# Kernel optimization log

Measured on AMD Instinct MI355X. Metric: run time of the kernel, lower is better.

Reference implementation:

```python
import jax, jax.numpy as jnp
import numpy as np

D = 64        # inner_feature_len (dim)
HID = 128     # hidden_channels of the edge MLP
NCONV = 2     # n_conv
STEPS = 3     # Set2Set processing_steps
NSEG = 128    # number of graphs in the batch


def setup_inputs() -> dict:
    key = jax.random.key(0)
    ks = jax.random.split(key, 30)
    N, E, FN, FE = 10000, 64000, 92, 41
    s = 0.05
    p = lambda i, shape: jax.random.normal(ks[i], shape, jnp.float32) * s
    return {
        "x": jax.random.normal(ks[0], (N, FN), jnp.float32),
        "edge_attr": jax.random.uniform(ks[1], (E, FE), dtype=jnp.float32),
        "lin0_w": p(2, (D, FN)), "lin0_b": p(3, (D,)),
        "nn1_w": p(4, (HID, FE)), "nn1_b": p(5, (HID,)),
        "nn2_w": p(6, (D * D, HID)), "nn2_b": p(7, (D * D,)),
        "root_w": p(8, (D, D)), "conv_b": p(9, (D,)),
        "gru_w_ih": p(10, (3 * D, D)), "gru_w_hh": p(11, (3 * D, D)),
        "gru_b_ih": p(12, (3 * D,)), "gru_b_hh": p(13, (3 * D,)),
        "lstm_w_ih": p(14, (4 * D, 2 * D)), "lstm_w_hh": p(15, (4 * D, D)),
        "lstm_b_ih": p(16, (4 * D,)), "lstm_b_hh": p(17, (4 * D,)),
        "lin1_w": p(18, (D, 2 * D)), "lin1_b": p(19, (D,)),
        "lin2_w": p(20, (1, D)), "lin2_b": p(21, (1,)),
        "edge_index": jax.random.randint(ks[22], (2, E), 0, N, dtype=jnp.int32),
        "batch": jnp.sort(jax.random.randint(ks[23], (N,), 0, NSEG, dtype=jnp.int32)),
    }


def _gru_step(m, h, w_ih, w_hh, b_ih, b_hh):
    # torch GRU gate order: r, z, n
    gi = m @ w_ih.T + b_ih
    gh = h @ w_hh.T + b_hh
    r = jax.nn.sigmoid(gi[:, :D] + gh[:, :D])
    z = jax.nn.sigmoid(gi[:, D:2 * D] + gh[:, D:2 * D])
    n = jnp.tanh(gi[:, 2 * D:] + r * gh[:, 2 * D:])
    return (1.0 - z) * n + z * h


def _forward(x, edge_attr, lin0_w, lin0_b, nn1_w, nn1_b, nn2_w, nn2_b, root_w, conv_b,
             gru_w_ih, gru_w_hh, gru_b_ih, gru_b_hh, lstm_w_ih, lstm_w_hh, lstm_b_ih,
             lstm_b_hh, lin1_w, lin1_b, lin2_w, lin2_b, edge_index, batch):
    N = x.shape[0]
    src, dst = edge_index[0], edge_index[1]

    # Edge-conditioned weight matrices: [E, D, D] (dominant intermediate)
    We = (jax.nn.relu(edge_attr @ nn1_w.T + nn1_b) @ nn2_w.T + nn2_b).reshape(-1, D, D)
    deg = jnp.clip(jax.ops.segment_sum(jnp.ones_like(src, jnp.float32), dst, num_segments=N), 1.0, None)

    out = jax.nn.relu(x @ lin0_w.T + lin0_b)   # [N, D]
    h = out                                     # GRU hidden (num_layers=1)
    for _ in range(NCONV):
        # NNConv: gather -> per-edge matmul -> scatter-mean, plus root transform + bias
        msg = jnp.einsum('ei,eio->eo', out[src], We)                 # [E, D]
        agg = jax.ops.segment_sum(msg, dst, num_segments=N) / deg[:, None]
        m = jax.nn.relu(agg + out @ root_w.T + conv_b)
        h = _gru_step(m, h, gru_w_ih, gru_w_hh, gru_b_ih, gru_b_hh)
        out = h

    # Set2Set pooling (LSTM-attention readout)
    q_star = jnp.zeros((NSEG, 2 * D), x.dtype)
    hl = jnp.zeros((NSEG, D), x.dtype)
    cl = jnp.zeros((NSEG, D), x.dtype)
    for _ in range(STEPS):
        g = q_star @ lstm_w_ih.T + lstm_b_ih + hl @ lstm_w_hh.T + lstm_b_hh
        i = jax.nn.sigmoid(g[:, :D])
        f = jax.nn.sigmoid(g[:, D:2 * D])
        gg = jnp.tanh(g[:, 2 * D:3 * D])
        o = jax.nn.sigmoid(g[:, 3 * D:])
        cl = f * cl + i * gg
        hl = o * jnp.tanh(cl)
        q = hl                                   # [NSEG, D]
        e = jnp.sum(out * q[batch], axis=-1)     # [N]
        mmax = jax.ops.segment_max(e, batch, num_segments=NSEG)
        a = jnp.exp(e - mmax[batch])
        denom = jax.ops.segment_sum(a, batch, num_segments=NSEG)
        a = a / denom[batch]
        r = jax.ops.segment_sum(a[:, None] * out, batch, num_segments=NSEG)  # [NSEG, D]
        q_star = jnp.concatenate([q, r], axis=1)

    y = jax.nn.relu(q_star @ lin1_w.T + lin1_b) @ lin2_w.T + lin2_b
    return y.reshape(-1)


def reference(x, edge_attr, lin0_w, lin0_b, nn1_w, nn1_b, nn2_w, nn2_b, root_w, conv_b,
              gru_w_ih, gru_w_hh, gru_b_ih, gru_b_hh, lstm_w_ih, lstm_w_hh, lstm_b_ih,
              lstm_b_hh, lin1_w, lin1_b, lin2_w, lin2_b, edge_index, batch):
    return _forward(x, edge_attr, lin0_w, lin0_b, nn1_w, nn1_b, nn2_w, nn2_b, root_w,
                    conv_b, gru_w_ih, gru_w_hh, gru_b_ih, gru_b_hh, lstm_w_ih, lstm_w_hh,
                    lstm_b_ih, lstm_b_hh, lin1_w, lin1_b, lin2_w, lin2_b, edge_index, batch)
```

## Files before the change

kernel.cpp:

```cpp
#include <hip/hip_runtime.h>
#include <hip/hip_bf16.h>
#include <math.h>

#define DD 64
#define HIDC 128
#define FN 92
#define FE 41
#define S2CAP 192

typedef unsigned short u16;
typedef short bf16x8 __attribute__((ext_vector_type(8)));
typedef float f32x4 __attribute__((ext_vector_type(4)));
typedef u16 u16x8 __attribute__((ext_vector_type(8)));

__device__ __forceinline__ float sigmoidf_(float x){ return 1.f/(1.f+expf(-x)); }

__device__ __forceinline__ u16 f2bf(float v){
  union { float f; unsigned u; } x; x.f = v;
  unsigned r = x.u + 0x7fff + ((x.u >> 16) & 1);
  return (u16)(r >> 16);
}
__device__ __forceinline__ float bf2f(u16 v){
  union { float f; unsigned u; } x; x.u = ((unsigned)v) << 16;
  return x.f;
}
__device__ __forceinline__ void split_bf(float v, u16& h, u16& l){
  h = f2bf(v); l = f2bf(v - bf2f(h));
}

__global__ void k_pack(const float* __restrict__ lin0_w, const float* __restrict__ nn1_w,
                       const float* __restrict__ root_w, const float* __restrict__ gwih,
                       const float* __restrict__ gwhh, const float* __restrict__ lwih,
                       const float* __restrict__ lwhh, const float* __restrict__ lin1_w,
                       float* __restrict__ lin0T, float* __restrict__ nn1T,
                       float* __restrict__ rootT, float* __restrict__ wihT,
                       float* __restrict__ whhT, float* __restrict__ lwihT,
                       float* __restrict__ lwhhT, float* __restrict__ lin1T)
{
  int idx = blockIdx.x*blockDim.x + threadIdx.x;
  if (idx < 92*64){ int k=idx/64, o=idx%64; lin0T[k*64+o] = lin0_w[o*92+k]; return; } idx -= 92*64;
  if (idx < 41*128){ int k=idx/128, h=idx%128; nn1T[k*128+h] = nn1_w[h*41+k]; return; } idx -= 41*128;
  if (idx < 64*64){ int i=idx/64, o=idx%64; rootT[i*64+o] = root_w[o*64+i]; return; } idx -= 64*64;
  if (idx < 64*192){ int i=idx/192, g=idx%192; wihT[i*192+g] = gwih[g*64+i]; return; } idx -= 64*192;
  if (idx < 64*192){ int i=idx/192, g=idx%192; whhT[i*192+g] = gwhh[g*64+i]; return; } idx -= 64*192;
  if (idx < 128*256){ int j=idx/256, t=idx%256; lwihT[j*256+t] = lwih[t*128+j]; return; } idx -= 128*256;
  if (idx < 64*256){ int j=idx/256, t=idx%256; lwhhT[j*256+t] = lwhh[t*64+j]; return; } idx -= 64*256;
  if (idx < 128*64){ int j=idx/64, t=idx%64; lin1T[j*64+t] = lin1_w[t*128+j]; return; }
}

__global__ void k_pack_b2(const float* __restrict__ nn2_w,
                          u16* __restrict__ BhT, u16* __restrict__ BlT){
  int idx = blockIdx.x*256 + threadIdx.x;
  if (idx >= 524288) return;
  int i  = idx & 63;
  int ho = (idx >> 6) & 4095;
  int c  = idx >> 18;
  int h = ho >> 6, o = ho & 63;
  float v = nn2_w[(size_t)(i*64+o)*128 + c*64 + h];
  u16 hi, lo; split_bf(v, hi, lo);
  BhT[idx] = hi; BlT[idx] = lo;
}

__global__ void k_pack_b1(const float* __restrict__ nn1_w,
                          u16* __restrict__ BT1h, u16* __restrict__ BT1l){
  int idx = blockIdx.x*256 + threadIdx.x;
  if (idx >= 8192) return;
  int h = idx >> 6, k = idx & 63;
  float v = (k < FE) ? nn1_w[(size_t)h*FE + k] : 0.f;
  u16 hi, lo; split_bf(v, hi, lo);
  BT1h[idx] = hi; BT1l[idx] = lo;
}

__global__ void k_split_ea(const float* __restrict__ ea, const int* __restrict__ sortedE,
                           u16* __restrict__ eaH, u16* __restrict__ eaL, int E){
  int idx = blockIdx.x*256 + threadIdx.x;
  if (idx >= E*64) return;
  int ew = idx >> 6, k = idx & 63;
  int e = sortedE[ew];
  float v = (k < FE) ? ea[(size_t)e*FE + k] : 0.f;
  u16 hi, lo; split_bf(v, hi, lo);
  eaH[idx] = hi; eaL[idx] = lo;
}

__global__ __launch_bounds__(256) void k_node_mlp(const float* __restrict__ x,
    const float* __restrict__ lin0T, const float* __restrict__ lin0_b,
    const float* __restrict__ nn2_b,
    float* __restrict__ out, u16* __restrict__ outH, u16* __restrict__ outL,
    float* __restrict__ bterm, int N)
{
  __shared__ float xs[16][FN];
  const int w = threadIdx.x>>6, o = threadIdx.x&63;
  const int nb = blockIdx.x*16 + w*4;
  for (int idx = o; idx < 4*FN; idx += 64){
    int j = idx/FN, k = idx%FN;
    int n = nb + j;
    xs[w*4+j][k] = (n<N) ? x[(size_t)n*FN + k] : 0.f;
  }
  float acc[4];
  float bv = lin0_b[o];
  #pragma unroll
  for (int j=0;j<4;j++) acc[j] = bv;
  for (int k=0;k<FN;k++){
    float lw = lin0T[k*64+o];
    #pragma unroll
    for (int j=0;j<4;j++) acc[j] = fmaf(xs[w*4+j][k], lw, acc[j]);
  }
  float v[4];
  #pragma unroll
  for (int j=0;j<4;j++){
    v[j] = fmaxf(acc[j], 0.f);
    int n = nb + j;
    if (n < N){
      out[(size_t)n*64+o] = v[j];
      u16 hi, lo; split_bf(v[j], hi, lo);
      outH[(size_t)n*64+o] = hi;
      outL[(size_t)n*64+o] = lo;
    }
  }
  float bt[4] = {0.f,0.f,0.f,0.f};
  for (int i=0;i<64;i++){
    float wnb = nn2_b[i*64+o];
    #pragma unroll
    for (int j=0;j<4;j++) bt[j] = fmaf(__shfl(v[j], i, 64), wnb, bt[j]);
  }
  #pragma unroll
  for (int j=0;j<4;j++){
    int n = nb + j;
    if (n < N) bterm[(size_t)n*64+o] = bt[j];
  }
}

__global__ void k_count(const int* __restrict__ dst, const int* __restrict__ src,
                        float* __restrict__ deg, int* __restrict__ scnt, int E){
  int e = blockIdx.x*blockDim.x + threadIdx.x;
  if (e < E){
    atomicAdd(&deg[dst[e]], 1.f);
    atomicAdd(&scnt[src[e]], 1);
  }
}

__global__ void k_scan1(const int* __restrict__ cnt, int* __restrict__ excl,
                        int* __restrict__ bsum, int N){
  __shared__ int buf[256];
  int i = blockIdx.x*256 + threadIdx.x;
  int v = (i<N) ? cnt[i] : 0;
  buf[threadIdx.x] = v;
  __syncthreads();
  #pragma unroll
  for (int off=1; off<256; off<<=1){
    int t = (threadIdx.x>=off) ? buf[threadIdx.x-off] : 0;
    __syncthreads();
    buf[threadIdx.x] += t;
    __syncthreads();
  }
  if (i<N) excl[i] = buf[threadIdx.x] - v;
  if (threadIdx.x==255) bsum[blockIdx.x] = buf[255];
}
__global__ void k_scan2(int* __restrict__ bsum, int nb){
  __shared__ int buf[256];
  int v = (threadIdx.x<nb) ? bsum[threadIdx.x] : 0;
  buf[threadIdx.x] = v;
  __syncthreads();
  #pragma unroll
  for (int off=1; off<256; off<<=1){
    int t = (threadIdx.x>=off) ? buf[threadIdx.x-off] : 0;
    __syncthreads();
    buf[threadIdx.x] += t;
    __syncthreads();
  }
  if (threadIdx.x<nb) bsum[threadIdx.x] = buf[threadIdx.x] - v;
}
__global__ void k_scan3(int* __restrict__ starts, int* __restrict__ cursor,
                        const int* __restrict__ bsum, int N, int E){
  int i = blockIdx.x*256 + threadIdx.x;
  if (i<N){
    int s = starts[i] + bsum[blockIdx.x];
    starts[i] = s;
    cursor[i] = s;
  }
  if (i==0) starts[N] = E;
}

__global__ void k_sort(const int* __restrict__ src, const int* __restrict__ dst,
                       int* __restrict__ cursor, int* __restrict__ sortedE,
                       int* __restrict__ dstS, int E){
  int e = blockIdx.x*256 + threadIdx.x;
  if (e < E){
    int s = src[e];
    int p = atomicAdd(&cursor[s], 1);
    sortedE[p] = e;
    dstS[p] = dst[e];
  }
}

__global__ __launch_bounds__(256,3) void k_edge_mlp_mfma(
    const u16* __restrict__ eaH, const u16* __restrict__ eaL,
    const u16* __restrict__ BT1h, const u16* __restrict__ BT1l,
    const float* __restrict__ nn1_b, float* __restrict__ hidden, int E)
{
  const int lane = threadIdx.x & 63;
  const int wave = threadIdx.x >> 6;
  const int row  = lane & 15;
  const int quad = lane >> 4;
  const int m0 = blockIdx.x*128 + (wave>>1)*64;
  const int n0 = (wave&1)*64;

  bf16x8 AH0[4], AH1[4], AL0[4], AL1[4];
  #pragma unroll
  for (int p=0;p<4;p++){
    int ar = min(m0 + p*16 + row, E-1);
    const u16* aH = eaH + (size_t)ar*64 + quad*8;
    const u16* aL = eaL + (size_t)ar*64 + quad*8;
    AH0[p] = *(const bf16x8*)(aH);
    AH1[p] = *(const bf16x8*)(aH + 32);
    AL0[p] = *(const bf16x8*)(aL);
    AL1[p] = *(const bf16x8*)(aL + 32);
  }
  #pragma unroll
  for (int tb=0;tb<4;tb++){
    const u16* bH = BT1h + (size_t)(n0 + tb*16 + row)*64 + quad*8;
    const u16* bL = BT1l + (size_t)(n0 + tb*16 + row)*64 + quad*8;
    bf16x8 bh0 = *(const bf16x8*)(bH);
    bf16x8 bh1 = *(const bf16x8*)(bH + 32);
    bf16x8 bl0 = *(const bf16x8*)(bL);
    bf16x8 bl1 = *(const bf16x8*)(bL + 32);
    float4 bias;
    {
      int nb = n0 + tb*16 + quad*4;
      bias.x = nn1_b[nb+0]; bias.y = nn1_b[nb+1];
      bias.z = nn1_b[nb+2]; bias.w = nn1_b[nb+3];
    }
    #pragma unroll
    for (int ta=0;ta<4;ta++){
      f32x4 a = {0.f,0.f,0.f,0.f};
      a = __builtin_amdgcn_mfma_f32_16x16x32_bf16(bh0, AH0[ta], a, 0,0,0);
      a = __builtin_amdgcn_mfma_f32_16x16x32_bf16(bh1, AH1[ta], a, 0,0,0);
      a = __builtin_amdgcn_mfma_f32_16x16x32_bf16(bl0, AH0[ta], a, 0,0,0);
      a = __builtin_amdgcn_mfma_f32_16x16x32_bf16(bl1, AH1[ta], a, 0,0,0);
      a = __builtin_amdgcn_mfma_f32_16x16x32_bf16(bh0, AL0[ta], a, 0,0,0);
      a = __builtin_amdgcn_mfma_f32_16x16x32_bf16(bh1, AL1[ta], a, 0,0,0);
      int m = m0 + ta*16 + row;
      if (m < E){
        float4 v;
        v.x = fmaxf(a[0]+bias.x, 0.f); v.y = fmaxf(a[1]+bias.y, 0.f);
        v.z = fmaxf(a[2]+bias.z, 0.f); v.w = fmaxf(a[3]+bias.w, 0.f);
        *(float4*)(hidden + (size_t)m*128 + n0 + tb*16 + quad*4) = v;
      }
    }
  }
}

__global__ __launch_bounds__(256,4) void k_qgemm_mfma(
    const u16* __restrict__ Ah, const u16* __restrict__ Al,
    const u16* __restrict__ BhT, const u16* __restrict__ BlT,
    u16* __restrict__ C, int M, int cbase)
{
  const int lane = threadIdx.x & 63;
  const int wave = threadIdx.x >> 6;
  const int row  = lane & 15;
  const int quad = lane >> 4;
  const int m0 = blockIdx.y * 32;
  const int col = cbase + blockIdx.x * 256 + wave * 64;
  const int chunk = col >> 12;
  const int n0 = col & 4095;
  const u16* Bh = BhT + (size_t)chunk*262144;
  const u16* Bl = BlT + (size_t)chunk*262144;

  bf16x8 AH0[2], AH1[2], AL0[2], AL1[2];
  #pragma unroll
  for (int p=0;p<2;p++){
    int ar = min(m0 + p*16 + row, M-1);
    const u16* aH = Ah + (size_t)ar*64 + quad*8;
    const u16* aL = Al + (size_t)ar*64 + quad*8;
    AH0[p] = *(const bf16x8*)(aH);
    AH1[p] = *(const bf16x8*)(aH + 32);
    AL0[p] = *(const bf16x8*)(aL);
    AL1[p] = *(const bf16x8*)(aL + 32);
  }

  f32x4 acc[2][4];
  #pragma unroll
  for (int ta=0;ta<2;ta++)
    #pragma unroll
    for (int tb=0;tb<4;tb++)
      acc[ta][tb] = (f32x4){0.f,0.f,0.f,0.f};

  #pragma unroll
  for (int tb=0;tb<4;tb++){
    const u16* bH = Bh + (size_t)(n0 + tb*16 + row)*64 + quad*8;
    const u16* bL = Bl + (size_t)(n0 + tb*16 + row)*64 + quad*8;
    bf16x8 bh0 = *(const bf16x8*)(bH);
    bf16x8 bh1 = *(const bf16x8*)(bH + 32);
    bf16x8 bl0 = *(const bf16x8*)(bL);
    bf16x8 bl1 = *(const bf16x8*)(bL + 32);
    #pragma unroll
    for (int ta=0;ta<2;ta++){
      f32x4 a = acc[ta][tb];
      a = __builtin_amdgcn_mfma_f32_16x16x32_bf16(bh0, AH0[ta], a, 0,0,0);
      a = __builtin_amdgcn_mfma_f32_16x16x32_bf16(bh1, AH1[ta], a, 0,0,0);
      a = __builtin_amdgcn_mfma_f32_16x16x32_bf16(bl0, AH0[ta], a, 0,0,0);
      a = __builtin_amdgcn_mfma_f32_16x16x32_bf16(bl1, AH1[ta], a, 0,0,0);
      a = __builtin_amdgcn_mfma_f32_16x16x32_bf16(bh0, AL0[ta], a, 0,0,0);
      a = __builtin_amdgcn_mfma_f32_16x16x32_bf16(bh1, AL1[ta], a, 0,0,0);
      acc[ta][tb] = a;
    }
  }

  const int cbl = (col - cbase) >> 6;
  #pragma unroll
  for (int ta=0;ta<2;ta++){
    int m = m0 + ta*16 + row;
    if (m >= M) continue;
    u16* dst = C + ((size_t)cbl*M + m)*64 + quad*8;
    #pragma unroll
    for (int p=0;p<2;p++){
      f32x4 aa = acc[ta][2*p];
      f32x4 ab = acc[ta][2*p+1];
      u16x8 v;
      v[0]=f2bf(aa[0]); v[1]=f2bf(aa[1]); v[2]=f2bf(aa[2]); v[3]=f2bf(aa[3]);
      v[4]=f2bf(ab[0]); v[5]=f2bf(ab[1]); v[6]=f2bf(ab[2]); v[7]=f2bf(ab[3]);
      __builtin_nontemporal_store(v, (u16x8*)(dst + p*32));
    }
  }
}

__global__ __launch_bounds__(256) void k_edge_gather(const u16* __restrict__ Q,
    const float* __restrict__ hidden, int h0, int cb0, int addbt,
    const float* __restrict__ bterm, const int* __restrict__ starts,
    const int* __restrict__ dstS, float* __restrict__ agg, int N)
{
  __shared__ float hs[4][64];
  __shared__ float red[4][64];
  const int wv = threadIdx.x>>6, lane = threadIdx.x&63;
  const int n = blockIdx.x*4 + wv;
  if (n >= N) return;
  const int e0 = starts[n], e1 = starts[n+1];
  if (e0 >= e1) return;
  const int sg = lane>>4, oq = lane&15;
  const int posb = ((oq>>3)<<5) + ((oq&3)<<3) + (((oq>>2)&1)<<2);
  const u16* qp = Q + ((size_t)(cb0+sg)*N + n)*64 + posb;
  const size_t jstride = (size_t)N*256;
  ushort4 qreg[16];
  #pragma unroll
  for (int j=0;j<16;j++) qreg[j] = *(const ushort4*)(qp + (size_t)j*jstride);
  const float bt = addbt ? bterm[(size_t)n*64 + lane] : 0.f;

  float hvN = hidden[(size_t)e0*128 + h0 + lane];
  int   dN  = dstS[e0];
  for (int e=e0; e<e1; ++e){
    const float hv = hvN;
    const int   d  = dN;
    if (e+1 < e1){
      hvN = hidden[(size_t)(e+1)*128 + h0 + lane];
      dN  = dstS[e+1];
    }
    hs[wv][lane] = hv;
    float a0=0.f,a1=0.f,a2=0.f,a3=0.f;
    #pragma unroll
    for (int j=0;j<16;j++){
      float h4 = hs[wv][j*4+sg];
      a0 = fmaf(h4, bf2f(qreg[j].x), a0);
      a1 = fmaf(h4, bf2f(qreg[j].y), a1);
      a2 = fmaf(h4, bf2f(qreg[j].z), a2);
      a3 = fmaf(h4, bf2f(qreg[j].w), a3);
    }
    a0 += __shfl_xor(a0,16); a0 += __shfl_xor(a0,32);
    a1 += __shfl_xor(a1,16); a1 += __shfl_xor(a1,32);
    a2 += __shfl_xor(a2,16); a2 += __shfl_xor(a2,32);
    a3 += __shfl_xor(a3,16); a3 += __shfl_xor(a3,32);
    if (lane < 16){
      float4 r; r.x=a0; r.y=a1; r.z=a2; r.w=a3;
      *(float4*)&red[wv][lane*4] = r;
    }
    atomicAdd(&agg[(size_t)d*64 + lane], bt + red[wv][lane]);
  }
}

__global__ __launch_bounds__(256) void k_node_update(const float* __restrict__ outOld,
    const float* __restrict__ agg, const float* __restrict__ deg,
    const float* __restrict__ rootT, const float* __restrict__ conv_b,
    const float* __restrict__ wihT, const float* __restrict__ whhT,
    const float* __restrict__ b_ih, const float* __restrict__ b_hh,
    const float* __restrict__ nn2_b,
    float* __restrict__ outNew, u16* __restrict__ outH, u16* __restrict__ outL,
    float* __restrict__ bterm, int N)
{
  __shared__ float hs[16][64];
  __shared__ float ms[16][64];
  const int w = threadIdx.x>>6, o = threadIdx.x&63;
  const int nb = blockIdx.x*16 + w*4;
  float h[4];
  #pragma unroll
  for (int j=0;j<4;j++){
    int n = nb+j;
    h[j] = (n<N) ? outOld[(size_t)n*64+o] : 0.f;
    hs[w*4+j][o] = h[j];
  }
  float root[4] = {0.f,0.f,0.f,0.f};
  for (int i=0;i<64;i++){
    float rw = rootT[i*64+o];
    #pragma unroll
    for (int j=0;j<4;j++) root[j] = fmaf(hs[w*4+j][i], rw, root[j]);
  }
  float cb = conv_b[o];
  float m[4];
  #pragma unroll
  for (int j=0;j<4;j++){
    int n = nb+j;
    float d = (n<N) ? fmaxf(deg[n], 1.f) : 1.f;
    float a = (n<N) ? agg[(size_t)n*64+o]/d : 0.f;
    m[j] = fmaxf(a + root[j] + cb, 0.f);
    ms[w*4+j][o] = m[j];
  }
  float gir[4],giz[4],gin[4],ghr[4],ghz[4],ghn[4];
  float bir=b_ih[o], biz=b_ih[64+o], bin=b_ih[128+o];
  float bhr=b_hh[o], bhz=b_hh[64+o], bhn=b_hh[128+o];
  #pragma unroll
  for (int j=0;j<4;j++){
    gir[j]=bir; giz[j]=biz; gin[j]=bin;
    ghr[j]=bhr; ghz[j]=bhz; ghn[j]=bhn;
  }
  for (int i=0;i<64;i++){
    float wr=wihT[i*192+o], wz=wihT[i*192+64+o], wn=wihT[i*192+128+o];
    float vr=whhT[i*192+o], vz=whhT[i*192+64+o], vn=whhT[i*192+128+o];
    #pragma unroll
    for (int j=0;j<4;j++){
      float mi = ms[w*4+j][i], hi = hs[w*4+j][i];
      gir[j]=fmaf(mi,wr,gir[j]); giz[j]=fmaf(mi,wz,giz[j]); gin[j]=fmaf(mi,wn,gin[j]);
      ghr[j]=fmaf(hi,vr,ghr[j]); ghz[j]=fmaf(hi,vz,ghz[j]); ghn[j]=fmaf(hi,vn,ghn[j]);
    }
  }
  float v[4];
  #pragma unroll
  for (int j=0;j<4;j++){
    float r = sigmoidf_(gir[j]+ghr[j]);
    float z = sigmoidf_(giz[j]+ghz[j]);
    float nn = tanhf(gin[j] + r*ghn[j]);
    v[j] = (1.f-z)*nn + z*h[j];
    int n = nb+j;
    if (n<N){
      outNew[(size_t)n*64+o] = v[j];
      u16 hi16, lo16; split_bf(v[j], hi16, lo16);
      outH[(size_t)n*64+o] = hi16;
      outL[(size_t)n*64+o] = lo16;
    }
  }
  float bt[4] = {0.f,0.f,0.f,0.f};
  for (int i=0;i<64;i++){
    float wnb = nn2_b[i*64+o];
    #pragma unroll
    for (int j=0;j<4;j++) bt[j] = fmaf(__shfl(v[j], i, 64), wnb, bt[j]);
  }
  #pragma unroll
  for (int j=0;j<4;j++){
    int n = nb+j;
    if (n<N) bterm[(size_t)n*64+o] = bt[j];
  }
}

__global__ __launch_bounds__(256) void k_set2set(const float* __restrict__ out,
    const int* __restrict__ batch, int N,
    const float* __restrict__ lwihT, const float* __restrict__ lwhhT,
    const float* __restrict__ b_ih, const float* __restrict__ b_hh,
    const float* __restrict__ lin1T, const float* __restrict__ lin1_b,
    const float* __restrict__ lin2_w, const float* __restrict__ lin2_b,
    float* __restrict__ y)
{
  __shared__ float X[S2CAP][65];
  __shared__ float earr[S2CAP];
  __shared__ float qstar[128], hl[64], cl[64], g[256];
  __shared__ float rpart[4][64], spart[4], redm[4], zs[64];
  __shared__ int sb[2];
  const int tid = threadIdx.x;
  const int b = blockIdx.x;
  const int wid = tid>>6, lane = tid&63;
  if (tid < 128) qstar[tid] = 0.f;
  if (tid < 64){ hl[tid]=0.f; cl[tid]=0.f; }
  if (tid == 0){
    int lo=0, hi=N;
    while (lo<hi){ int mid=(lo+hi)>>1; if (batch[mid] < b) lo=mid+1; else hi=mid; }
    sb[0]=lo;
    int lo2=lo, hi2=N;
    while (lo2<hi2){ int mid=(lo2+hi2)>>1; if (batch[mid] < b+1) lo2=mid+1; else hi2=mid; }
    sb[1]=lo2;
  }
  __syncthreads();
  const int nlo = sb[0], nhi = sb[1], nn = nhi - nlo;
  const bool single = (nn <= S2CAP);
  if (single){
    for (int idx = tid; idx < nn*64; idx += 256){
      X[idx>>6][idx&63] = out[(size_t)(nlo + (idx>>6))*64 + (idx&63)];
    }
  }
  __syncthreads();

  for (int step=0; step<3; step++){
    float gs = b_ih[tid] + b_hh[tid];
    for (int j=0;j<128;j++) gs = fmaf(qstar[j], lwihT[j*256+tid], gs);
    for (int j=0;j<64;j++)  gs = fmaf(hl[j],    lwhhT[j*256+tid], gs);
    g[tid] = gs;
    __syncthreads();
    if (tid < 64){
      float ig = sigmoidf_(g[tid]);
      float fg = sigmoidf_(g[64+tid]);
      float gg = tanhf(g[128+tid]);
      float og = sigmoidf_(g[192+tid]);
      float c = fg*cl[tid] + ig*gg;
      cl[tid] = c;
      hl[tid] = og*tanhf(c);
    }
    __syncthreads();

    if (single){
      float lm = -INFINITY;
      for (int n = tid; n < nn; n += 256){
        float acc = 0.f;
        #pragma unroll 8
        for (int d=0; d<64; d++) acc = fmaf(X[n][d], hl[d], acc);
        earr[n] = acc;
        lm = fmaxf(lm, acc);
      }
      lm = fmaxf(lm, __shfl_xor(lm,1));  lm = fmaxf(lm, __shfl_xor(lm,2));
      lm = fmaxf(lm, __shfl_xor(lm,4));  lm = fmaxf(lm, __shfl_xor(lm,8));
      lm = fmaxf(lm, __shfl_xor(lm,16)); lm = fmaxf(lm, __shfl_xor(lm,32));
      if (lane==0) redm[wid] = lm;
      __syncthreads();
      if (tid==0) redm[0] = fmaxf(fmaxf(redm[0],redm[1]), fmaxf(redm[2],redm[3]));
      __syncthreads();
      const float gmax = redm[0];
      float ls = 0.f;
      for (int n = tid; n < nn; n += 256){
        float a = expf(earr[n] - gmax);
        earr[n] = a;
        ls += a;
      }
      ls += __shfl_xor(ls,1);  ls += __shfl_xor(ls,2);  ls += __shfl_xor(ls,4);
      ls += __shfl_xor(ls,8);  ls += __shfl_xor(ls,16); ls += __shfl_xor(ls,32);
      if (lane==0) spart[wid] = ls;
      __syncthreads();
      float racc = 0.f;
      for (int n = wid; n < nn; n += 4) racc = fmaf(earr[n], X[n][lane], racc);
      rpart[wid][lane] = racc;
      __syncthreads();
      if (tid < 64){
        float r = rpart[0][tid]+rpart[1][tid]+rpart[2][tid]+rpart[3][tid];
        float s = spart[0]+spart[1]+spart[2]+spart[3];
        qstar[tid] = hl[tid];
        qstar[64+tid] = (nn>0) ? r/s : 0.f;
      }
      __syncthreads();
    } else {
      float qv = hl[lane];
      float lm = -INFINITY;
      for (int n = nlo + wid; n < nhi; n += 4){
        float p = out[(size_t)n*64 + lane]*qv;
        p += __shfl_xor(p,1); p += __shfl_xor(p,2); p += __shfl_xor(p,4);
        p += __shfl_xor(p,8); p += __shfl_xor(p,16); p += __shfl_xor(p,32);
        lm = fmaxf(lm, p);
      }
      if (lane==0) redm[wid] = lm;
      __syncthreads();
      if (tid==0) redm[0] = fmaxf(fmaxf(redm[0],redm[1]), fmaxf(redm[2],redm[3]));
      __syncthreads();
      float gmax = redm[0];
      float sw = 0.f, racc = 0.f;
      for (int n = nlo + wid; n < nhi; n += 4){
        float ol = out[(size_t)n*64 + lane];
        float p = ol*qv;
        p += __shfl_xor(p,1); p += __shfl_xor(p,2); p += __shfl_xor(p,4);
        p += __shfl_xor(p,8); p += __shfl_xor(p,16); p += __shfl_xor(p,32);
        float a = expf(p - gmax);
        sw += a;
        racc = fmaf(a, ol, racc);
      }
      rpart[wid][lane] = racc;
      if (lane==0) spart[wid] = sw;
      __syncthreads();
      if (tid < 64){
        float r = rpart[0][tid]+rpart[1][tid]+rpart[2][tid]+rpart[3][tid];
        float s = spart[0]+spart[1]+spart[2]+spart[3];
        qstar[tid] = hl[tid];
        qstar[64+tid] = (nn>0) ? r/s : 0.f;
      }
      __syncthreads();
    }
  }
  if (tid < 64){
    float acc = lin1_b[tid];
    for (int j=0;j<128;j++) acc = fmaf(qstar[j], lin1T[j*64+tid], acc);
    zs[tid] = fmaxf(acc, 0.f);
  }
  __syncthreads();
  if (tid < 64){
    float v = zs[lane]*lin2_w[lane];
    v += __shfl_xor(v,1); v += __shfl_xor(v,2); v += __shfl_xor(v,4);
    v += __shfl_xor(v,8); v += __shfl_xor(v,16); v += __shfl_xor(v,32);
    if (lane==0) y[b] = v + lin2_b[0];
  }
}

extern "C" void kernel_launch(void* const* d_in, const int* in_sizes, int n_in,
                              void* d_out, int out_size, void* d_ws, size_t ws_size,
                              hipStream_t stream)
{
  const float* x      = (const float*)d_in[0];
  const float* eattr  = (const float*)d_in[1];
  const float* lin0_w = (const float*)d_in[2];
  const float* lin0_b = (const float*)d_in[3];
  const float* nn1_w  = (const float*)d_in[4];
  const float* nn1_b  = (const float*)d_in[5];
  const float* nn2_w  = (const float*)d_in[6];
  const float* nn2_b  = (const float*)d_in[7];
  const float* root_w = (const float*)d_in[8];
  const float* conv_b = (const float*)d_in[9];
  const float* gwih   = (const float*)d_in[10];
  const float* gwhh   = (const float*)d_in[11];
  const float* gbih   = (const float*)d_in[12];
  const float* gbhh   = (const float*)d_in[13];
  const float* lwih   = (const float*)d_in[14];
  const float* lwhh   = (const float*)d_in[15];
  const float* lbih   = (const float*)d_in[16];
  const float* lbhh   = (const float*)d_in[17];
  const float* lin1_w = (const float*)d_in[18];
  const float* lin1_b = (const float*)d_in[19];
  const float* lin2_w = (const float*)d_in[20];
  const float* lin2_b = (const float*)d_in[21];
  const int*   eidx   = (const int*)d_in[22];
  const int*   batch  = (const int*)d_in[23];

  const int N = in_sizes[0]/FN;
  const int E = in_sizes[1]/FE;
  const int* srcI = eidx;
  const int* dstI = eidx + E;

  char* w = (char*)d_ws;
  size_t off = 0;
  auto alloc = [&](size_t bytes)->char* {
    char* p = w + off;
    off = (off + bytes + 255) & ~(size_t)255;
    return p;
  };
  float* degw  = (float*)alloc((size_t)N*4);
  int*   scnt  = (int*)alloc((size_t)N*4);
  int*   starts= (int*)alloc((size_t)(N+1)*4);
  int*   cursor= (int*)alloc((size_t)N*4);
  int*   bsum  = (int*)alloc((size_t)256*4);
  int*   sortedE=(int*)alloc((size_t)E*4);
  int*   dstS  = (int*)alloc((size_t)E*4);
  float* outA  = (float*)alloc((size_t)N*64*4);
  float* outB  = (float*)alloc((size_t)N*64*4);
  u16*   outAH = (u16*)alloc((size_t)N*64*2);
  u16*   outAL = (u16*)alloc((size_t)N*64*2);
  u16*   outBH = (u16*)alloc((size_t)N*64*2);
  u16*   outBL = (u16*)alloc((size_t)N*64*2);
  float* agg   = (float*)alloc((size_t)N*64*4);
  float* bterm = (float*)alloc((size_t)N*64*4);
  float* hidden= (float*)alloc((size_t)E*128*4);
  u16*   B2hT  = (u16*)alloc((size_t)524288*2);
  u16*   B2lT  = (u16*)alloc((size_t)524288*2);
  u16*   BT1h  = (u16*)alloc((size_t)8192*2);
  u16*   BT1l  = (u16*)alloc((size_t)8192*2);
  float* lin0T = (float*)alloc((size_t)92*64*4);
  float* nn1T  = (float*)alloc((size_t)41*128*4);
  float* rootT = (float*)alloc((size_t)64*64*4);
  float* wihT  = (float*)alloc((size_t)64*192*4);
  float* whhT  = (float*)alloc((size_t)64*192*4);
  float* lwihT = (float*)alloc((size_t)128*256*4);
  float* lwhhT = (float*)alloc((size_t)64*256*4);
  float* lin1T = (float*)alloc((size_t)128*64*4);

  size_t qbig = (size_t)N*8192*2;
  size_t qsmall = (size_t)N*4096*2;
  bool merged = (ws_size - off) >= (qbig + 512);
  u16* Q = (u16*)alloc(merged ? qbig : qsmall);
  u16* eaH = (u16*)Q;
  u16* eaL = eaH + (size_t)E*64;

  const int NB = (N+255)/256;

  hipMemsetAsync(degw, 0, (size_t)N*4, stream);
  hipMemsetAsync(scnt, 0, (size_t)N*4, stream);
  k_pack<<<(97152+255)/256, 256, 0, stream>>>(lin0_w, nn1_w, root_w, gwih, gwhh,
      lwih, lwhh, lin1_w, lin0T, nn1T, rootT, wihT, whhT, lwihT, lwhhT, lin1T);
  k_pack_b2<<<524288/256, 256, 0, stream>>>(nn2_w, B2hT, B2lT);
  k_pack_b1<<<8192/256, 256, 0, stream>>>(nn1_w, BT1h, BT1l);
  k_node_mlp<<<(N+15)/16, 256, 0, stream>>>(x, lin0T, lin0_b, nn2_b, outA, outAH, outAL, bterm, N);
  k_count<<<(E+255)/256, 256, 0, stream>>>(dstI, srcI, degw, scnt, E);
  k_scan1<<<NB, 256, 0, stream>>>(scnt, starts, bsum, N);
  k_scan2<<<1, 256, 0, stream>>>(bsum, NB);
  k_scan3<<<NB, 256, 0, stream>>>(starts, cursor, bsum, N, E);
  k_sort<<<(E+255)/256, 256, 0, stream>>>(srcI, dstI, cursor, sortedE, dstS, E);
  k_split_ea<<<((size_t)E*64+255)/256, 256, 0, stream>>>(eattr, sortedE, eaH, eaL, E);
  k_edge_mlp_mfma<<<(E+127)/128, 256, 0, stream>>>(eaH, eaL, BT1h, BT1l, nn1_b, hidden, E);

  float* cur = outA; float* nxt = outB;
  u16* curH = outAH; u16* curL = outAL;
  u16* nxtH = outBH; u16* nxtL = outBL;
  const int gatherG = (N+3)/4;
  for (int conv=0; conv<2; conv++){
    hipMemsetAsync(agg, 0, (size_t)N*64*4, stream);
    if (merged){
      k_qgemm_mfma<<<dim3(32,(N+31)/32), 256, 0, stream>>>(curH, curL, B2hT, B2lT, Q, N, 0);
      k_edge_gather<<<gatherG, 256, 0, stream>>>(Q, hidden, 0,  0,  1, bterm, starts, dstS, agg, N);
      k_edge_gather<<<gatherG, 256, 0, stream>>>(Q, hidden, 64, 64, 0, bterm, starts, dstS, agg, N);
    } else {
      for (int c=0; c<2; c++){
        k_qgemm_mfma<<<dim3(16,(N+31)/32), 256, 0, stream>>>(curH, curL, B2hT, B2lT, Q, N, c*4096);
        k_edge_gather<<<gatherG, 256, 0, stream>>>(Q, hidden, c*64, 0, (c==0)?1:0, bterm, starts, dstS, agg, N);
      }
    }
    k_node_update<<<(N+15)/16, 256, 0, stream>>>(cur, agg, degw, rootT, conv_b,
        wihT, whhT, gbih, gbhh, nn2_b, nxt, nxtH, nxtL, bterm, N);
    float* t = cur; cur = nxt; nxt = t;
    u16* th = curH; curH = nxtH; nxtH = th;
    u16* tl = curL; curL = nxtL; nxtL = tl;
  }

  k_set2set<<<128, 256, 0, stream>>>(cur, batch, N, lwihT, lwhhT, lbih, lbhh,
      lin1T, lin1_b, lin2_w, lin2_b, (float*)d_out);
}
```

Baseline: 667.8 us.

## Fuse per-node Q GEMM with edge gather in a single conv kernel

Replaces the separate Q GEMM, which wrote a large bf16 Q tensor of N×8192 to global memory, and the two edge-gather kernels with one fused kernel. Each block computes Q for 32 source nodes chunk by chunk in shared memory and accumulates per-edge messages in LDS. The hidden edge activations are stored transposed so the fused kernel can read them coalesced per channel. This removes the large Q round trip through HBM. In exchange it uses about 120KB of LDS per block, which allows one block per CU, and it adds many syncthreads and an imbalanced per-node edge loop. The edge-MLP epilogue now writes scattered strided stores.

```diff
diff --git a/kernel.cpp b/kernel.cpp
--- a/kernel.cpp
+++ b/kernel.cpp
@@ -7,6 +7,8 @@
 #define FN 92
 #define FE 41
 #define S2CAP 192
+#define NPB 32
+#define ECAP 320
 
 typedef unsigned short u16;
 typedef short bf16x8 __attribute__((ext_vector_type(8)));
@@ -196,7 +198,7 @@
 __global__ __launch_bounds__(256,3) void k_edge_mlp_mfma(
     const u16* __restrict__ eaH, const u16* __restrict__ eaL,
     const u16* __restrict__ BT1h, const u16* __restrict__ BT1l,
-    const float* __restrict__ nn1_b, float* __restrict__ hidden, int E)
+    const float* __restrict__ nn1_b, float* __restrict__ hiddenT, int E)
 {
   const int lane = threadIdx.x & 63;
   const int wave = threadIdx.x >> 6;
@@ -241,138 +243,147 @@
       a = __builtin_amdgcn_mfma_f32_16x16x32_bf16(bh1, AL1[ta], a, 0,0,0);
       int m = m0 + ta*16 + row;
       if (m < E){
-        float4 v;
-        v.x = fmaxf(a[0]+bias.x, 0.f); v.y = fmaxf(a[1]+bias.y, 0.f);
-        v.z = fmaxf(a[2]+bias.z, 0.f); v.w = fmaxf(a[3]+bias.w, 0.f);
-        *(float4*)(hidden + (size_t)m*128 + n0 + tb*16 + quad*4) = v;
-      }
-    }
-  }
-}
-
-__global__ __launch_bounds__(256,4) void k_qgemm_mfma(
+        int colb = n0 + tb*16 + quad*4;
+        hiddenT[(size_t)(colb+0)*E + m] = fmaxf(a[0]+bias.x, 0.f);
+        hiddenT[(size_t)(colb+1)*E + m] = fmaxf(a[1]+bias.y, 0.f);
+        hiddenT[(size_t)(colb+2)*E + m] = fmaxf(a[2]+bias.z, 0.f);
+        hiddenT[(size_t)(colb+3)*E + m] = fmaxf(a[3]+bias.w, 0.f);
+      }
+    }
+  }
+}
+
+__global__ __launch_bounds__(256,1) void k_fused_conv(
     const u16* __restrict__ Ah, const u16* __restrict__ Al,
     const u16* __restrict__ BhT, const u16* __restrict__ BlT,
-    u16* __restrict__ C, int M, int cbase)
+    const float* __restrict__ hiddenT, const float* __restrict__ bterm,
+    const int* __restrict__ starts, const int* __restrict__ dstS,
+    float* __restrict__ agg, int N, int E)
 {
-  const int lane = threadIdx.x & 63;
-  const int wave = threadIdx.x >> 6;
-  const int row  = lane & 15;
-  const int quad = lane >> 4;
-  const int m0 = blockIdx.y * 32;
-  const int col = cbase + blockIdx.x * 256 + wave * 64;
-  const int chunk = col >> 12;
-  const int n0 = col & 4095;
-  const u16* Bh = BhT + (size_t)chunk*262144;
-  const u16* Bl = BlT + (size_t)chunk*262144;
+  __shared__ float Qs[4][32][68];
+  __shared__ float msg[ECAP][64];
+  __shared__ float hst[4][ECAP];
+  const int tid  = threadIdx.x;
+  const int wv   = tid >> 6, lane = tid & 63;
+  const int row  = lane & 15, quad = lane >> 4;
+  const int n0g  = blockIdx.x * NPB;
 
   bf16x8 AH0[2], AH1[2], AL0[2], AL1[2];
   #pragma unroll
-  for (int p=0;p<2;p++){
-    int ar = min(m0 + p*16 + row, M-1);
+  for (int ta=0;ta<2;ta++){
+    int ar = min(n0g + ta*16 + row, N-1);
     const u16* aH = Ah + (size_t)ar*64 + quad*8;
     const u16* aL = Al + (size_t)ar*64 + quad*8;
-    AH0[p] = *(const bf16x8*)(aH);
-    AH1[p] = *(const bf16x8*)(aH + 32);
-    AL0[p] = *(const bf16x8*)(aL);
-    AL1[p] = *(const bf16x8*)(aL + 32);
-  }
-
-  f32x4 acc[2][4];
-  #pragma unroll
-  for (int ta=0;ta<2;ta++)
-    #pragma unroll
-    for (int tb=0;tb<4;tb++)
-      acc[ta][tb] = (f32x4){0.f,0.f,0.f,0.f};
-
-  #pragma unroll
-  for (int tb=0;tb<4;tb++){
-    const u16* bH = Bh + (size_t)(n0 + tb*16 + row)*64 + quad*8;
-    const u16* bL = Bl + (size_t)(n0 + tb*16 + row)*64 + quad*8;
-    bf16x8 bh0 = *(const bf16x8*)(bH);
-    bf16x8 bh1 = *(const bf16x8*)(bH + 32);
-    bf16x8 bl0 = *(const bf16x8*)(bL);
-    bf16x8 bl1 = *(const bf16x8*)(bL + 32);
-    #pragma unroll
-    for (int ta=0;ta<2;ta++){
-      f32x4 a = acc[ta][tb];
-      a = __builtin_amdgcn_mfma_f32_16x16x32_bf16(bh0, AH0[ta], a, 0,0,0);
-      a = __builtin_amdgcn_mfma_f32_16x16x32_bf16(bh1, AH1[ta], a, 0,0,0);
-      a = __builtin_amdgcn_mfma_f32_16x16x32_bf16(bl0, AH0[ta], a, 0,0,0);
-      a = __builtin_amdgcn_mfma_f32_16x16x32_bf16(bl1, AH1[ta], a, 0,0,0);
-      a = __builtin_amdgcn_mfma_f32_16x16x32_bf16(bh0, AL0[ta], a, 0,0,0);
-      a = __builtin_amdgcn_mfma_f32_16x16x32_bf16(bh1, AL1[ta], a, 0,0,0);
-      acc[ta][tb] = a;
-    }
-  }
-
-  const int cbl = (col - cbase) >> 6;
-  #pragma unroll
-  for (int ta=0;ta<2;ta++){
-    int m = m0 + ta*16 + row;
-    if (m >= M) continue;
-    u16* dst = C + ((size_t)cbl*M + m)*64 + quad*8;
-    #pragma unroll
-    for (int p=0;p<2;p++){
-      f32x4 aa = acc[ta][2*p];
-      f32x4 ab = acc[ta][2*p+1];
-      u16x8 v;
-      v[0]=f2bf(aa[0]); v[1]=f2bf(aa[1]); v[2]=f2bf(aa[2]); v[3]=f2bf(aa[3]);
-      v[4]=f2bf(ab[0]); v[5]=f2bf(ab[1]); v[6]=f2bf(ab[2]); v[7]=f2bf(ab[3]);
-      __builtin_nontemporal_store(v, (u16x8*)(dst + p*32));
-    }
-  }
-}
-
-__global__ __launch_bounds__(256) void k_edge_gather(const u16* __restrict__ Q,
-    const float* __restrict__ hidden, int h0, int cb0, int addbt,
-    const float* __restrict__ bterm, const int* __restrict__ starts,
-    const int* __restrict__ dstS, float* __restrict__ agg, int N)
-{
-  __shared__ float hs[4][64];
-  __shared__ float red[4][64];
-  const int wv = threadIdx.x>>6, lane = threadIdx.x&63;
-  const int n = blockIdx.x*4 + wv;
-  if (n >= N) return;
-  const int e0 = starts[n], e1 = starts[n+1];
-  if (e0 >= e1) return;
-  const int sg = lane>>4, oq = lane&15;
-  const int posb = ((oq>>3)<<5) + ((oq&3)<<3) + (((oq>>2)&1)<<2);
-  const u16* qp = Q + ((size_t)(cb0+sg)*N + n)*64 + posb;
-  const size_t jstride = (size_t)N*256;
-  ushort4 qreg[16];
-  #pragma unroll
-  for (int j=0;j<16;j++) qreg[j] = *(const ushort4*)(qp + (size_t)j*jstride);
-  const float bt = addbt ? bterm[(size_t)n*64 + lane] : 0.f;
-
-  float hvN = hidden[(size_t)e0*128 + h0 + lane];
-  int   dN  = dstS[e0];
-  for (int e=e0; e<e1; ++e){
-    const float hv = hvN;
-    const int   d  = dN;
-    if (e+1 < e1){
-      hvN = hidden[(size_t)(e+1)*128 + h0 + lane];
-      dN  = dstS[e+1];
-    }
-    hs[wv][lane] = hv;
-    float a0=0.f,a1=0.f,a2=0.f,a3=0.f;
-    #pragma unroll
-    for (int j=0;j<16;j++){
-      float h4 = hs[wv][j*4+sg];
-      a0 = fmaf(h4, bf2f(qreg[j].x), a0);
-      a1 = fmaf(h4, bf2f(qreg[j].y), a1);
-      a2 = fmaf(h4, bf2f(qreg[j].z), a2);
-      a3 = fmaf(h4, bf2f(qreg[j].w), a3);
-    }
-    a0 += __shfl_xor(a0,16); a0 += __shfl_xor(a0,32);
-    a1 += __shfl_xor(a1,16); a1 += __shfl_xor(a1,32);
-    a2 += __shfl_xor(a2,16); a2 += __shfl_xor(a2,32);
-    a3 += __shfl_xor(a3,16); a3 += __shfl_xor(a3,32);
-    if (lane < 16){
-      float4 r; r.x=a0; r.y=a1; r.z=a2; r.w=a3;
-      *(float4*)&red[wv][lane*4] = r;
-    }
-    atomicAdd(&agg[(size_t)d*64 + lane], bt + red[wv][lane]);
+    AH0[ta] = *(const bf16x8*)(aH);
+    AH1[ta] = *(const bf16x8*)(aH + 32);
+    AL0[ta] = *(const bf16x8*)(aL);
+    AL1[ta] = *(const bf16x8*)(aL + 32);
+  }
+
+  const int eblk0 = starts[n0g];
+  const int eblk1 = starts[min(n0g + NPB, N)];
+
+  for (int ce0 = eblk0; ce0 < eblk1; ce0 += ECAP){
+    const int cnt = min(ECAP, eblk1 - ce0);
+    const int ce1 = ce0 + cnt;
+    for (int i = tid; i < cnt*64; i += 256) (&msg[0][0])[i] = 0.f;
+    int eS[8], eE[8];
+    #pragma unroll
+    for (int nn=0;nn<8;nn++){
+      int n = n0g + wv*8 + nn;
+      if (n < N){
+        eS[nn] = max(starts[n], ce0);
+        eE[nn] = min(starts[n+1], ce1);
+      } else { eS[nn] = 0; eE[nn] = 0; }
+    }
+    float hr0[4], hr1[4];
+    #pragma unroll
+    for (int j=0;j<4;j++){
+      hr0[j] = (tid < cnt)       ? hiddenT[(size_t)j*E + ce0 + tid]       : 0.f;
+      hr1[j] = (tid + 256 < cnt) ? hiddenT[(size_t)j*E + ce0 + tid + 256] : 0.f;
+    }
+    __syncthreads();
+
+    for (int g=0; g<32; ++g){
+      const int cb = g*4 + wv;
+      const u16* Bh = BhT + ((size_t)(cb>>6))*262144 + (size_t)(cb&63)*4096;
+      const u16* Bl = BlT + ((size_t)(cb>>6))*262144 + (size_t)(cb&63)*4096;
+      f32x4 acc[2][4];
+      #pragma unroll
+      for (int ta=0;ta<2;ta++)
+        #pragma unroll
+        for (int tb=0;tb<4;tb++)
+          acc[ta][tb] = (f32x4){0.f,0.f,0.f,0.f};
+      #pragma unroll
+      for (int tb=0;tb<4;tb++){
+        const u16* bH = Bh + (size_t)(tb*16 + row)*64 + quad*8;
+        const u16* bL = Bl + (size_t)(tb*16 + row)*64 + quad*8;
+        bf16x8 bh0 = *(const bf16x8*)(bH);
+        bf16x8 bh1 = *(const bf16x8*)(bH + 32);
+        bf16x8 bl0 = *(const bf16x8*)(bL);
+        bf16x8 bl1 = *(const bf16x8*)(bL + 32);
+        #pragma unroll
+        for (int ta=0;ta<2;ta++){
+          f32x4 a = acc[ta][tb];
+          a = __builtin_amdgcn_mfma_f32_16x16x32_bf16(bh0, AH0[ta], a, 0,0,0);
+          a = __builtin_amdgcn_mfma_f32_16x16x32_bf16(bh1, AH1[ta], a, 0,0,0);
+          a = __builtin_amdgcn_mfma_f32_16x16x32_bf16(bl0, AH0[ta], a, 0,0,0);
+          a = __builtin_amdgcn_mfma_f32_16x16x32_bf16(bl1, AH1[ta], a, 0,0,0);
+          a = __builtin_amdgcn_mfma_f32_16x16x32_bf16(bh0, AL0[ta], a, 0,0,0);
+          a = __builtin_amdgcn_mfma_f32_16x16x32_bf16(bh1, AL1[ta], a, 0,0,0);
+          acc[ta][tb] = a;
+        }
+      }
+      #pragma unroll
+      for (int ta=0;ta<2;ta++)
+        #pragma unroll
+        for (int tb=0;tb<4;tb++)
+          *(f32x4*)&Qs[wv][ta*16+row][tb*16+quad*4] = acc[ta][tb];
+      #pragma unroll
+      for (int j=0;j<4;j++){
+        if (tid < cnt)       hst[j][tid]     = hr0[j];
+        if (tid + 256 < cnt) hst[j][tid+256] = hr1[j];
+      }
+      if (g < 31){
+        const size_t hb = (size_t)(g+1)*4;
+        #pragma unroll
+        for (int j=0;j<4;j++){
+          hr0[j] = (tid < cnt)       ? hiddenT[(hb+j)*E + ce0 + tid]       : 0.f;
+          hr1[j] = (tid + 256 < cnt) ? hiddenT[(hb+j)*E + ce0 + tid + 256] : 0.f;
+        }
+      }
+      __syncthreads();
+      #pragma unroll
+      for (int nn=0;nn<8;nn++){
+        const int es = eS[nn], ee = eE[nn];
+        if (es >= ee) continue;
+        const int nl = wv*8 + nn;
+        const float q0 = Qs[0][nl][lane];
+        const float q1 = Qs[1][nl][lane];
+        const float q2 = Qs[2][nl][lane];
+        const float q3 = Qs[3][nl][lane];
+        for (int e = es; e < ee; ++e){
+          const int el = e - ce0;
+          float m = msg[el][lane];
+          m = fmaf(hst[0][el], q0, m);
+          m = fmaf(hst[1][el], q1, m);
+          m = fmaf(hst[2][el], q2, m);
+          m = fmaf(hst[3][el], q3, m);
+          msg[el][lane] = m;
+        }
+      }
+      __syncthreads();
+    }
+    #pragma unroll
+    for (int nn=0;nn<8;nn++){
+      const int es = eS[nn], ee = eE[nn];
+      if (es >= ee) continue;
+      const int n = n0g + wv*8 + nn;
+      const float bt = bterm[(size_t)n*64 + lane];
+      for (int e = es; e < ee; ++e)
+        atomicAdd(&agg[(size_t)dstS[e]*64 + lane], bt + msg[e-ce0][lane]);
+    }
+    __syncthreads();
   }
 }
 
@@ -655,7 +666,9 @@
   u16*   outBL = (u16*)alloc((size_t)N*64*2);
   float* agg   = (float*)alloc((size_t)N*64*4);
   float* bterm = (float*)alloc((size_t)N*64*4);
-  float* hidden= (float*)alloc((size_t)E*128*4);
+  float* hiddenT=(float*)alloc((size_t)E*128*4);
+  u16*   eaH   = (u16*)alloc((size_t)E*64*2);
+  u16*   eaL   = (u16*)alloc((size_t)E*64*2);
   u16*   B2hT  = (u16*)alloc((size_t)524288*2);
   u16*   B2lT  = (u16*)alloc((size_t)524288*2);
   u16*   BT1h  = (u16*)alloc((size_t)8192*2);
@@ -668,13 +681,6 @@
   float* lwihT = (float*)alloc((size_t)128*256*4);
   float* lwhhT = (float*)alloc((size_t)64*256*4);
   float* lin1T = (float*)alloc((size_t)128*64*4);
-
-  size_t qbig = (size_t)N*8192*2;
-  size_t qsmall = (size_t)N*4096*2;
-  bool merged = (ws_size - off) >= (qbig + 512);
-  u16* Q = (u16*)alloc(merged ? qbig : qsmall);
-  u16* eaH = (u16*)Q;
-  u16* eaL = eaH + (size_t)E*64;
 
   const int NB = (N+255)/256;
 
@@ -691,24 +697,16 @@
   k_scan3<<<NB, 256, 0, stream>>>(starts, cursor, bsum, N, E);
   k_sort<<<(E+255)/256, 256, 0, stream>>>(srcI, dstI, cursor, sortedE, dstS, E);
   k_split_ea<<<((size_t)E*64+255)/256, 256, 0, stream>>>(eattr, sortedE, eaH, eaL, E);
-  k_edge_mlp_mfma<<<(E+127)/128, 256, 0, stream>>>(eaH, eaL, BT1h, BT1l, nn1_b, hidden, E);
+  k_edge_mlp_mfma<<<(E+127)/128, 256, 0, stream>>>(eaH, eaL, BT1h, BT1l, nn1_b, hiddenT, E);
 
   float* cur = outA; float* nxt = outB;
   u16* curH = outAH; u16* curL = outAL;
   u16* nxtH = outBH; u16* nxtL = outBL;
-  const int gatherG = (N+3)/4;
+  const int fusedG = (N + NPB - 1) / NPB;
   for (int conv=0; conv<2; conv++){
     hipMemsetAsync(agg, 0, (size_t)N*64*4, stream);
-    if (merged){
-      k_qgemm_mfma<<<dim3(32,(N+31)/32), 256, 0, stream>>>(curH, curL, B2hT, B2lT, Q, N, 0);
-      k_edge_gather<<<gatherG, 256, 0, stream>>>(Q, hidden, 0,  0,  1, bterm, starts, dstS, agg, N);
-      k_edge_gather<<<gatherG, 256, 0, stream>>>(Q, hidden, 64, 64, 0, bterm, starts, dstS, agg, N);
-    } else {
-      for (int c=0; c<2; c++){
-        k_qgemm_mfma<<<dim3(16,(N+31)/32), 256, 0, stream>>>(curH, curL, B2hT, B2lT, Q, N, c*4096);
-        k_edge_gather<<<gatherG, 256, 0, stream>>>(Q, hidden, c*64, 0, (c==0)?1:0, bterm, starts, dstS, agg, N);
-      }
-    }
+    k_fused_conv<<<fusedG, 256, 0, stream>>>(curH, curL, B2hT, B2lT, hiddenT,
+        bterm, starts, dstS, agg, N, E);
     k_node_update<<<(N+15)/16, 256, 0, stream>>>(cur, agg, degw, rootT, conv_b,
         wihT, whhT, gbih, gbhh, nn2_b, nxt, nxtH, nxtL, bterm, N);
     float* t = cur; cur = nxt; nxt = t;
```

Result: slower. 1.196 ms (+79.1%).
